# Kernel tuning notes

Hardware: AMD Instinct MI355X
Metric: run time of the kernel (lower is better)

## Reference

```python
import jax, jax.numpy as jnp
import numpy as np

DIMENSIONS = 10000
NUM_LEVELS = 21
N_GRAM_SIZE = 4
HIGH = 20.0
B, T, C, NUM_CLASSES = 4, 128, 32, 10


def _sign_hv(key, shape):
    # torchhd Random/Level MAP hypervectors are +-1 valued
    return jnp.where(jax.random.bernoulli(key, 0.5, shape), 1.0, -1.0).astype(jnp.float32)


def setup_inputs() -> dict:
    key = jax.random.key(0)
    k_x, k_sig, k_ch, k_ts, k_cls = jax.random.split(key, 5)
    x = jax.random.uniform(k_x, (B, T, C), dtype=jnp.float32) * HIGH  # raw signal values in [0, 20)
    signals_w = _sign_hv(k_sig, (NUM_LEVELS, DIMENSIONS))
    channels_w = _sign_hv(k_ch, (C, DIMENSIONS))  # unused in original math (dead bind), kept for parity
    timestamps_w = _sign_hv(k_ts, (T, DIMENSIONS))
    # original fills classify weight with 0.0; use small random so output is non-degenerate
    classify_w = jax.random.normal(k_cls, (NUM_CLASSES, DIMENSIONS), dtype=jnp.float32) * 0.01
    return {"x": x, "signals_w": signals_w, "channels_w": channels_w,
            "timestamps_w": timestamps_w, "classify_w": classify_w}


def reference(x, signals_w, channels_w, timestamps_w, classify_w):
    # Level embedding: map value in [0, HIGH] to nearest of NUM_LEVELS level hypervectors
    idx = jnp.clip(jnp.round(x / HIGH * (NUM_LEVELS - 1)), 0, NUM_LEVELS - 1).astype(jnp.int32)
    idx = jax.lax.stop_gradient(idx)
    signal = signals_w[idx]                                   # [B,T,C,D]
    # NOTE: bind with channels_w is dead code in the source (overwritten); omitted.
    samples = signal * timestamps_w[None, :, None, :]         # bind -> [B,T,C,D]
    samples = samples.sum(axis=2)                             # batch_bundle over channels -> [B,T,D]
    Tp = T - N_GRAM_SIZE + 1
    n_gram = None
    for i in range(N_GRAM_SIZE):
        sample = jnp.roll(samples[:, i:i + Tp], N_GRAM_SIZE - 1 - i, axis=-1)  # permute
        n_gram = sample if n_gram is None else n_gram * sample                  # bind
    sample_hv = n_gram.sum(axis=1)                            # batch_bundle over n-grams -> [B,D]
    enc = jnp.where(sample_hv > 0, 1.0, -1.0)                 # hard_quantize
    return enc @ classify_w.T                                 # [B,num_classes]
```

## Files before the change

### kernel.cpp

```cpp
#include <hip/hip_runtime.h>


#define D_ 10000
#define NL_ 21
#define B_ 4
#define T_ 128
#define C_ 32
#define NC_ 10
#define TD_ 80
#define NT_ 125
#define COLS_ (TD_ + 3)
#define CPAD_ 84

__global__ __launch_bounds__(256)
void hdc_fused(const float* __restrict__ x,
               const float* __restrict__ sig,
               const float* __restrict__ ts,
               const float* __restrict__ cw,
               float* __restrict__ out) {
    __shared__ float cnt[T_][NL_];
    __shared__ float sig_s[NL_][CPAD_];
    __shared__ float smp[T_][CPAD_];
    __shared__ float part_j[2 * TD_];
    __shared__ float part_k[4][NC_];

    const int tid   = threadIdx.x;
    const int b     = blockIdx.x / NT_;
    const int tile  = blockIdx.x % NT_;
    const int start = tile * TD_;

    for (int w = tid; w < T_ * NL_; w += 256) ((float*)cnt)[w] = 0.0f;
    __syncthreads();
    for (int w = tid; w < T_ * C_; w += 256) {
        float xv = x[b * T_ * C_ + w];
        float t2 = (xv / 20.0f) * 20.0f;
        float r  = rintf(t2);
        r = fminf(fmaxf(r, 0.0f), 20.0f);
        int lvl = (int)r;
        int t   = w >> 5;
        atomicAdd(&cnt[t][lvl], 1.0f);
    }
    for (int w = tid; w < NL_ * COLS_; w += 256) {
        int l = w / COLS_, col = w - l * COLS_;
        int dd = start - 3 + col; if (dd < 0) dd += D_;
        sig_s[l][col] = sig[l * D_ + dd];
    }
    __syncthreads();
    for (int w = tid; w < T_ * COLS_; w += 256) {
        int t = w / COLS_, col = w - t * COLS_;
        int dd = start - 3 + col; if (dd < 0) dd += D_;
        float acc = 0.0f;
        #pragma unroll
        for (int l = 0; l < NL_; ++l) acc += cnt[t][l] * sig_s[l][col];
        smp[t][col] = ts[t * D_ + dd] * acc;
    }
    __syncthreads();
    if (tid < 2 * TD_) {
        int od = tid >> 1, half = tid & 1;
        int j0 = half ? 63 : 0;
        int j1 = half ? 125 : 63;
        float acc = 0.0f;
        for (int j = j0; j < j1; ++j) {
            acc += smp[j][od] * smp[j + 1][od + 1] * smp[j + 2][od + 2] * smp[j + 3][od + 3];
        }
        part_j[tid] = acc;
    }
    __syncthreads();
    float enc = 0.0f;
    if (tid < TD_) {
        float tot = part_j[2 * tid] + part_j[2 * tid + 1];
        enc = (tot > 0.0f) ? 1.0f : -1.0f;
    }
    const int wave = tid >> 6;
    const int lane = tid & 63;
    #pragma unroll
    for (int k = 0; k < NC_; ++k) {
        float contrib = (tid < TD_) ? enc * cw[k * D_ + start + tid] : 0.0f;
        #pragma unroll
        for (int m = 32; m >= 1; m >>= 1) contrib += __shfl_xor(contrib, m, 64);
        if (lane == 0) part_k[wave][k] = contrib;
    }
    __syncthreads();
    if (tid < NC_) {
        float s = part_k[0][tid] + part_k[1][tid] + part_k[2][tid] + part_k[3][tid];
        atomicAdd(&out[b * NC_ + tid], s);
    }
}

extern "C" void kernel_launch(void* const* d_in, const int* in_sizes, int n_in,
                              void* d_out, int out_size, void* d_ws, size_t ws_size,
                              hipStream_t stream) {
    const float* x   = (const float*)d_in[0];
    const float* sig = (const float*)d_in[1];
    const float* ts  = (const float*)d_in[3];
    const float* cw  = (const float*)d_in[4];
    float* out = (float*)d_out;

    hipMemsetAsync(out, 0, (size_t)out_size * sizeof(float), stream);
    hdc_fused<<<B_ * NT_, 256, 0, stream>>>(x, sig, ts, cw, out);
}
```

Before: 109.6 us.

## Split histogram into pre-kernel and register-tile sample computation with smaller D tiles

```diff
diff --git a/kernel.cpp b/kernel.cpp
--- a/kernel.cpp
+++ b/kernel.cpp
@@ -1,89 +1,126 @@
 #include <hip/hip_runtime.h>
 
 
-#define D_ 10000
-#define NL_ 21
-#define B_ 4
-#define T_ 128
-#define C_ 32
-#define NC_ 10
-#define TD_ 80
-#define NT_ 125
-#define COLS_ (TD_ + 3)
-#define CPAD_ 84
+#define D_   10000
+#define NL_  21
+#define B_   4
+#define T_   128
+#define C_   32
+#define NC_  10
+#define TD_  50
+#define NT_  200
+#define CP_  56
+#define NCG_ 14
 
-__global__ __launch_bounds__(256)
-void hdc_fused(const float* __restrict__ x,
-               const float* __restrict__ sig,
-               const float* __restrict__ ts,
-               const float* __restrict__ cw,
-               float* __restrict__ out) {
-    __shared__ float cnt[T_][NL_];
-    __shared__ float sig_s[NL_][CPAD_];
-    __shared__ float smp[T_][CPAD_];
-    __shared__ float part_j[2 * TD_];
-    __shared__ float part_k[4][NC_];
+__global__ __launch_bounds__(128)
+void hist_kernel(const float* __restrict__ x, float* __restrict__ cnt) {
+    __shared__ float h[T_][NL_];
+    const int t = threadIdx.x;
+    const int b = blockIdx.x;
+    #pragma unroll
+    for (int l = 0; l < NL_; ++l) h[t][l] = 0.0f;
+    const float* xp = x + (b * T_ + t) * C_;
+    for (int c = 0; c < C_; ++c) {
+        float xv = xp[c];
+        float r  = rintf((xv / 20.0f) * 20.0f);
+        r = fminf(fmaxf(r, 0.0f), 20.0f);
+        h[t][(int)r] += 1.0f;
+    }
+    float* cp = cnt + (b * T_ + t) * NL_;
+    #pragma unroll
+    for (int l = 0; l < NL_; ++l) cp[l] = h[t][l];
+}
+
+__global__ __launch_bounds__(256, 3)
+void hdc_main(const float* __restrict__ sig,
+              const float* __restrict__ ts,
+              const float* __restrict__ cw,
+              const float* __restrict__ cnt,
+              float* __restrict__ out) {
+    __shared__ float cnt_s[T_][NL_];
+    __shared__ float smp[T_][CP_];
+    __shared__ float part[5 * TD_];
 
     const int tid   = threadIdx.x;
     const int b     = blockIdx.x / NT_;
     const int tile  = blockIdx.x % NT_;
     const int start = tile * TD_;
 
-    for (int w = tid; w < T_ * NL_; w += 256) ((float*)cnt)[w] = 0.0f;
-    __syncthreads();
-    for (int w = tid; w < T_ * C_; w += 256) {
-        float xv = x[b * T_ * C_ + w];
-        float t2 = (xv / 20.0f) * 20.0f;
-        float r  = rintf(t2);
-        r = fminf(fmaxf(r, 0.0f), 20.0f);
-        int lvl = (int)r;
-        int t   = w >> 5;
-        atomicAdd(&cnt[t][lvl], 1.0f);
-    }
-    for (int w = tid; w < NL_ * COLS_; w += 256) {
-        int l = w / COLS_, col = w - l * COLS_;
-        int dd = start - 3 + col; if (dd < 0) dd += D_;
-        sig_s[l][col] = sig[l * D_ + dd];
+    for (int w = tid; w < T_ * NL_; w += 256)
+        ((float*)cnt_s)[w] = cnt[b * T_ * NL_ + w];
+
+    const int  cg  = tid % NCG_;
+    const int  tch = tid / NCG_;
+    const bool act = tid < (NCG_ * 16);
+    const int  dd0 = start - 3 + cg * 4;
+    float sr[NL_][4];
+    if (act) {
+        #pragma unroll
+        for (int l = 0; l < NL_; ++l) {
+            #pragma unroll
+            for (int i = 0; i < 4; ++i) {
+                int dd = dd0 + i;
+                if (dd < 0) dd += D_;
+                if (dd >= D_) dd -= D_;
+                sr[l][i] = sig[l * D_ + dd];
+            }
+        }
     }
     __syncthreads();
-    for (int w = tid; w < T_ * COLS_; w += 256) {
-        int t = w / COLS_, col = w - t * COLS_;
-        int dd = start - 3 + col; if (dd < 0) dd += D_;
-        float acc = 0.0f;
-        #pragma unroll
-        for (int l = 0; l < NL_; ++l) acc += cnt[t][l] * sig_s[l][col];
-        smp[t][col] = ts[t * D_ + dd] * acc;
+
+    if (act) {
+        int d0 = dd0, d1 = dd0 + 1, d2 = dd0 + 2, d3 = dd0 + 3;
+        if (d0 < 0) d0 += D_;  if (d0 >= D_) d0 -= D_;
+        if (d1 < 0) d1 += D_;  if (d1 >= D_) d1 -= D_;
+        if (d2 < 0) d2 += D_;  if (d2 >= D_) d2 -= D_;
+        if (d3 < 0) d3 += D_;  if (d3 >= D_) d3 -= D_;
+        const int t0 = tch * 8;
+        for (int tt = 0; tt < 8; ++tt) {
+            const int t = t0 + tt;
+            const float* tp = ts + (size_t)t * D_;
+            float v0 = tp[d0], v1 = tp[d1], v2 = tp[d2], v3 = tp[d3];
+            float a0 = 0.f, a1 = 0.f, a2 = 0.f, a3 = 0.f;
+            #pragma unroll
+            for (int l = 0; l < NL_; ++l) {
+                float cv = cnt_s[t][l];
+                a0 += cv * sr[l][0];
+                a1 += cv * sr[l][1];
+                a2 += cv * sr[l][2];
+                a3 += cv * sr[l][3];
+            }
+            float4 r = make_float4(v0 * a0, v1 * a1, v2 * a2, v3 * a3);
+            *(float4*)&smp[t][cg * 4] = r;
+        }
     }
     __syncthreads();
-    if (tid < 2 * TD_) {
-        int od = tid >> 1, half = tid & 1;
-        int j0 = half ? 63 : 0;
-        int j1 = half ? 125 : 63;
+
+    if (tid < 5 * TD_) {
+        const int od = tid % TD_;
+        const int jc = tid / TD_;
+        const int j0 = jc * 25;
         float acc = 0.0f;
-        for (int j = j0; j < j1; ++j) {
+        #pragma unroll 5
+        for (int j = j0; j < j0 + 25; ++j) {
             acc += smp[j][od] * smp[j + 1][od + 1] * smp[j + 2][od + 2] * smp[j + 3][od + 3];
         }
-        part_j[tid] = acc;
+        part[tid] = acc;
     }
     __syncthreads();
-    float enc = 0.0f;
-    if (tid < TD_) {
-        float tot = part_j[2 * tid] + part_j[2 * tid + 1];
-        enc = (tot > 0.0f) ? 1.0f : -1.0f;
-    }
-    const int wave = tid >> 6;
-    const int lane = tid & 63;
-    #pragma unroll
-    for (int k = 0; k < NC_; ++k) {
-        float contrib = (tid < TD_) ? enc * cw[k * D_ + start + tid] : 0.0f;
+
+    if (tid < 64) {
+        float enc = 0.0f;
+        if (tid < TD_) {
+            float tot = part[tid] + part[tid + TD_] + part[tid + 2 * TD_]
+                      + part[tid + 3 * TD_] + part[tid + 4 * TD_];
+            enc = (tot > 0.0f) ? 1.0f : -1.0f;
+        }
         #pragma unroll
-        for (int m = 32; m >= 1; m >>= 1) contrib += __shfl_xor(contrib, m, 64);
-        if (lane == 0) part_k[wave][k] = contrib;
-    }
-    __syncthreads();
-    if (tid < NC_) {
-        float s = part_k[0][tid] + part_k[1][tid] + part_k[2][tid] + part_k[3][tid];
-        atomicAdd(&out[b * NC_ + tid], s);
+        for (int k = 0; k < NC_; ++k) {
+            float contrib = (tid < TD_) ? enc * cw[k * D_ + start + tid] : 0.0f;
+            #pragma unroll
+            for (int m = 32; m >= 1; m >>= 1) contrib += __shfl_xor(contrib, m, 64);
+            if (tid == 0) atomicAdd(&out[b * NC_ + k], contrib);
+        }
     }
 }
 
@@ -95,7 +132,9 @@
     const float* ts  = (const float*)d_in[3];
     const float* cw  = (const float*)d_in[4];
     float* out = (float*)d_out;
+    float* cnt = (float*)d_ws;
 
     hipMemsetAsync(out, 0, (size_t)out_size * sizeof(float), stream);
-    hdc_fused<<<B_ * NT_, 256, 0, stream>>>(x, sig, ts, cw, out);
+    hist_kernel<<<B_, T_, 0, stream>>>(x, cnt);
+    hdc_main<<<B_ * NT_, 256, 0, stream>>>(sig, ts, cw, cnt, out);
 }
```

Result: slower. 148.3 us (+35.3%).

## Split histogram into separate kernel and compute n-grams with wave shuffles

Applied to the files above, without the earlier changes.

```diff
diff --git a/kernel.cpp b/kernel.cpp
--- a/kernel.cpp
+++ b/kernel.cpp
@@ -1,89 +1,115 @@
 #include <hip/hip_runtime.h>
 
 
-#define D_ 10000
-#define NL_ 21
-#define B_ 4
-#define T_ 128
-#define C_ 32
-#define NC_ 10
-#define TD_ 80
-#define NT_ 125
-#define COLS_ (TD_ + 3)
-#define CPAD_ 84
+#define D_     10000
+#define NL_    21
+#define B_     4
+#define T_     128
+#define C_     32
+#define NC_    10
+#define OPW_   61
+#define NTILE_ 164
+
+__global__ __launch_bounds__(128)
+void hist_kernel(const float* __restrict__ x, float* __restrict__ cnt,
+                 float* __restrict__ out) {
+    const int t = threadIdx.x;
+    const int b = blockIdx.x;
+    if (b == 0 && t < B_ * NC_) out[t] = 0.0f;
+    float h[NL_];
+    #pragma unroll
+    for (int l = 0; l < NL_; ++l) h[l] = 0.0f;
+    const float* xp = x + (b * T_ + t) * C_;
+    #pragma unroll 8
+    for (int c = 0; c < C_; ++c) {
+        float r = rintf((xp[c] / 20.0f) * 20.0f);
+        r = fminf(fmaxf(r, 0.0f), 20.0f);
+        int lvl = (int)r;
+        #pragma unroll
+        for (int l = 0; l < NL_; ++l) h[l] += (l == lvl) ? 1.0f : 0.0f;
+    }
+    float* cp = cnt + (b * T_ + t) * NL_;
+    #pragma unroll
+    for (int l = 0; l < NL_; ++l) cp[l] = h[l];
+}
 
 __global__ __launch_bounds__(256)
-void hdc_fused(const float* __restrict__ x,
-               const float* __restrict__ sig,
-               const float* __restrict__ ts,
-               const float* __restrict__ cw,
-               float* __restrict__ out) {
-    __shared__ float cnt[T_][NL_];
-    __shared__ float sig_s[NL_][CPAD_];
-    __shared__ float smp[T_][CPAD_];
-    __shared__ float part_j[2 * TD_];
-    __shared__ float part_k[4][NC_];
+void hdc_main(const float* __restrict__ sig,
+              const float* __restrict__ ts,
+              const float* __restrict__ cw,
+              const float* __restrict__ cnt,
+              float* __restrict__ out) {
+    __shared__ float hv_s[4][64];
 
-    const int tid   = threadIdx.x;
-    const int b     = blockIdx.x / NT_;
-    const int tile  = blockIdx.x % NT_;
-    const int start = tile * TD_;
+    const int tid  = threadIdx.x;
+    const int lane = tid & 63;
+    const int w    = tid >> 6;
+    const int b    = blockIdx.x / NTILE_;
+    const int tile = blockIdx.x % NTILE_;
 
-    for (int w = tid; w < T_ * NL_; w += 256) ((float*)cnt)[w] = 0.0f;
+    int dcol = tile * OPW_ - 3 + lane;
+    if (dcol < 0)   dcol += D_;
+    if (dcol >= D_) dcol -= D_;
+
+    float sr[NL_];
+    #pragma unroll
+    for (int l = 0; l < NL_; ++l) sr[l] = sig[l * D_ + dcol];
+
+    int jo = (w == 0) ? 0 : (32 + 31 * (w - 1));
+    int nj = (w == 0) ? 32 : 31;
+    jo = __builtin_amdgcn_readfirstlane(jo);
+    nj = __builtin_amdgcn_readfirstlane(nj);
+
+    const float* cb = cnt + (b * T_ + jo) * NL_;
+    const float* tp = ts + (size_t)jo * D_ + dcol;
+
+    float a1 = 0.f, a2 = 0.f, a3 = 0.f, hv = 0.f;
+
+    #pragma unroll
+    for (int it = 0; it < 3; ++it) {
+        const float* cr = cb + it * NL_;
+        float s0 = 0.f, s1 = 0.f, s2 = 0.f;
+        #pragma unroll
+        for (int l = 0; l < 7; ++l) {
+            s0 += cr[l]      * sr[l];
+            s1 += cr[l + 7]  * sr[l + 7];
+            s2 += cr[l + 14] * sr[l + 14];
+        }
+        float a0 = tp[(size_t)it * D_] * ((s0 + s1) + s2);
+        a3 = a2; a2 = a1; a1 = a0;
+    }
+    #pragma unroll 4
+    for (int j = 0; j < nj; ++j) {
+        const int it = j + 3;
+        const float* cr = cb + it * NL_;
+        float s0 = 0.f, s1 = 0.f, s2 = 0.f;
+        #pragma unroll
+        for (int l = 0; l < 7; ++l) {
+            s0 += cr[l]      * sr[l];
+            s1 += cr[l + 7]  * sr[l + 7];
+            s2 += cr[l + 14] * sr[l + 14];
+        }
+        float a0 = tp[(size_t)it * D_] * ((s0 + s1) + s2);
+        float m3 = __shfl_up(a3, 3);
+        float m2 = __shfl_up(a2, 2);
+        float m1 = __shfl_up(a1, 1);
+        hv += m3 * m2 * m1 * a0;
+        a3 = a2; a2 = a1; a1 = a0;
+    }
+
+    hv_s[w][lane] = hv;
     __syncthreads();
-    for (int w = tid; w < T_ * C_; w += 256) {
-        float xv = x[b * T_ * C_ + w];
-        float t2 = (xv / 20.0f) * 20.0f;
-        float r  = rintf(t2);
-        r = fminf(fmaxf(r, 0.0f), 20.0f);
-        int lvl = (int)r;
-        int t   = w >> 5;
-        atomicAdd(&cnt[t][lvl], 1.0f);
-    }
-    for (int w = tid; w < NL_ * COLS_; w += 256) {
-        int l = w / COLS_, col = w - l * COLS_;
-        int dd = start - 3 + col; if (dd < 0) dd += D_;
-        sig_s[l][col] = sig[l * D_ + dd];
-    }
-    __syncthreads();
-    for (int w = tid; w < T_ * COLS_; w += 256) {
-        int t = w / COLS_, col = w - t * COLS_;
-        int dd = start - 3 + col; if (dd < 0) dd += D_;
-        float acc = 0.0f;
-        #pragma unroll
-        for (int l = 0; l < NL_; ++l) acc += cnt[t][l] * sig_s[l][col];
-        smp[t][col] = ts[t * D_ + dd] * acc;
-    }
-    __syncthreads();
-    if (tid < 2 * TD_) {
-        int od = tid >> 1, half = tid & 1;
-        int j0 = half ? 63 : 0;
-        int j1 = half ? 125 : 63;
-        float acc = 0.0f;
-        for (int j = j0; j < j1; ++j) {
-            acc += smp[j][od] * smp[j + 1][od + 1] * smp[j + 2][od + 2] * smp[j + 3][od + 3];
-        }
-        part_j[tid] = acc;
-    }
-    __syncthreads();
-    float enc = 0.0f;
-    if (tid < TD_) {
-        float tot = part_j[2 * tid] + part_j[2 * tid + 1];
-        enc = (tot > 0.0f) ? 1.0f : -1.0f;
-    }
-    const int wave = tid >> 6;
-    const int lane = tid & 63;
-    #pragma unroll
-    for (int k = 0; k < NC_; ++k) {
-        float contrib = (tid < TD_) ? enc * cw[k * D_ + start + tid] : 0.0f;
+
+    float tot = hv_s[0][lane] + hv_s[1][lane] + hv_s[2][lane] + hv_s[3][lane];
+    const int  dout  = tile * OPW_ + lane - 3;
+    const bool valid = (lane >= 3) && (dout < D_);
+    float enc = valid ? ((tot > 0.f) ? 1.f : -1.f) : 0.f;
+
+    for (int k = w; k < NC_; k += 4) {
+        float contrib = valid ? enc * cw[k * D_ + dout] : 0.f;
         #pragma unroll
         for (int m = 32; m >= 1; m >>= 1) contrib += __shfl_xor(contrib, m, 64);
-        if (lane == 0) part_k[wave][k] = contrib;
-    }
-    __syncthreads();
-    if (tid < NC_) {
-        float s = part_k[0][tid] + part_k[1][tid] + part_k[2][tid] + part_k[3][tid];
-        atomicAdd(&out[b * NC_ + tid], s);
+        if (lane == 0) atomicAdd(&out[b * NC_ + k], contrib);
     }
 }
 
@@ -95,7 +121,8 @@
     const float* ts  = (const float*)d_in[3];
     const float* cw  = (const float*)d_in[4];
     float* out = (float*)d_out;
+    float* cnt = (float*)d_ws;
 
-    hipMemsetAsync(out, 0, (size_t)out_size * sizeof(float), stream);
-    hdc_fused<<<B_ * NT_, 256, 0, stream>>>(x, sig, ts, cw, out);
+    hist_kernel<<<B_, T_, 0, stream>>>(x, cnt, out);
+    hdc_main<<<B_ * NTILE_, 256, 0, stream>>>(sig, ts, cw, cnt, out);
 }
```

Result: slower. 127.4 us (+16.3%).
